# Kernel tuning notes

Measured on AMD Instinct MI355X. Metric: run time of the kernel, lower is better.

The kernel has to match this reference:

```python
import jax, jax.numpy as jnp
import numpy as np
from jax import lax

RATIOS = np.array([0.5, 1.0, 2.0], dtype=np.float32)
SCALES = np.array([8.0, 16.0, 32.0], dtype=np.float32)
BASE = 16.0
FEAT_STRIDE = 16
N_PRE_NMS = 6000
N_POST_NMS = 300
NMS_THRESH = 0.7
MIN_SIZE = 16.0
SCALE = 1.0
NEG_INF = -1e30


def generate_anchor_base():
    # (y1, x1, y2, x2) anchors centered at (BASE/2, BASE/2)
    h = BASE * SCALES[None, :] * np.sqrt(RATIOS)[:, None]          # [3,3]
    w = BASE * SCALES[None, :] * np.sqrt(1.0 / RATIOS)[:, None]
    cy = cx = BASE / 2.0
    ab = np.stack([cy - h / 2, cx - w / 2, cy + h / 2, cx + w / 2], axis=-1)
    return jnp.asarray(ab.reshape(-1, 4), dtype=jnp.float32)       # [9,4]


def enumerate_shift_anchor(anchor_base, hh, ww):
    sy = jnp.arange(hh, dtype=jnp.float32) * FEAT_STRIDE
    sx = jnp.arange(ww, dtype=jnp.float32) * FEAT_STRIDE
    mx, my = jnp.meshgrid(sx, sy)                                   # np.meshgrid(shift_x, shift_y)
    shift = jnp.stack([my.ravel(), mx.ravel(), my.ravel(), mx.ravel()], axis=1)  # [K,4]
    return (shift[:, None, :] + anchor_base[None, :, :]).reshape(-1, 4)          # [K*9,4]


def conv2d(x, w, b, pad):
    y = lax.conv_general_dilated(x, w, (1, 1), [(pad, pad), (pad, pad)],
                                 dimension_numbers=('NCHW', 'OIHW', 'NCHW'))
    return y + b[None, :, None, None]


def loc2bbox(anchor, loc):
    h = anchor[:, 2] - anchor[:, 0]
    w = anchor[:, 3] - anchor[:, 1]
    cy = anchor[:, 0] + 0.5 * h
    cx = anchor[:, 1] + 0.5 * w
    dy, dx, dh, dw = loc[:, 0], loc[:, 1], loc[:, 2], loc[:, 3]
    ncy = dy * h + cy
    ncx = dx * w + cx
    nh = jnp.exp(dh) * h
    nw = jnp.exp(dw) * w
    return jnp.stack([ncy - 0.5 * nh, ncx - 0.5 * nw, ncy + 0.5 * nh, ncx + 0.5 * nw], axis=1)


def nms_fixed(boxes, scores):
    # boxes [P,4] already score-sorted desc; greedy NMS, fixed N_POST_NMS outputs (zero-padded)
    def body(i, state):
        sc, keep = state
        idx = jnp.argmax(sc)
        valid = sc[idx] > NEG_INF / 2
        keep = keep.at[i].set(jnp.where(valid, idx, -1))
        box = boxes[idx]
        tl = jnp.maximum(box[:2], boxes[:, :2])
        br = jnp.minimum(box[2:], boxes[:, 2:])
        wh = jnp.clip(br - tl, 0.0)
        inter = wh[:, 0] * wh[:, 1]
        a1 = (box[2] - box[0]) * (box[3] - box[1])
        a2 = (boxes[:, 2] - boxes[:, 0]) * (boxes[:, 3] - boxes[:, 1])
        iou = inter / jnp.maximum(a1 + a2 - inter, 1e-6)
        sc = jnp.where(iou > NMS_THRESH, NEG_INF, sc)
        sc = sc.at[idx].set(NEG_INF)
        return sc, keep
    keep = jnp.full((N_POST_NMS,), -1, dtype=jnp.int32)
    _, keep = lax.fori_loop(0, N_POST_NMS, body, (scores, keep))
    rois = boxes[jnp.maximum(keep, 0)]
    return jnp.where(keep[:, None] >= 0, rois, 0.0)                # [N_POST,4]


def propose_one(loc, fg_score, anchor, img_h, img_w):
    roi = loc2bbox(anchor, loc)                                     # [A,4]
    roi = jnp.stack([jnp.clip(roi[:, 0], 0.0, img_h),
                     jnp.clip(roi[:, 1], 0.0, img_w),
                     jnp.clip(roi[:, 2], 0.0, img_h),
                     jnp.clip(roi[:, 3], 0.0, img_w)], axis=1)
    min_size = MIN_SIZE * SCALE
    hs = roi[:, 2] - roi[:, 0]
    ws = roi[:, 3] - roi[:, 1]
    valid = (hs >= min_size) & (ws >= min_size)
    sc = jnp.where(valid, fg_score, NEG_INF)
    top_sc, top_idx = lax.top_k(sc, N_PRE_NMS)
    return nms_fixed(roi[top_idx], top_sc)


def reference(x, conv1_w, conv1_b, score_w, score_b, loc_w, loc_b, img_h, img_w):
    n, _, hh, ww = x.shape
    anchor = enumerate_shift_anchor(generate_anchor_base(), hh, ww)  # [hh*ww*9,4]
    n_anchor = anchor.shape[0] // (hh * ww)
    feat = jax.nn.relu(conv2d(x, conv1_w, conv1_b, 1))
    rpn_locs = conv2d(feat, loc_w, loc_b, 0).transpose(0, 2, 3, 1).reshape(n, -1, 4)
    rpn_scores = conv2d(feat, score_w, score_b, 0).transpose(0, 2, 3, 1)
    soft = jax.nn.softmax(rpn_scores.reshape(n, hh, ww, n_anchor, 2), axis=4)
    rpn_fg = soft[..., 1].reshape(n, -1)
    rpn_scores = rpn_scores.reshape(n, -1, 2)
    rois = jax.vmap(lambda l, s: propose_one(l, s, anchor, float(img_h), float(img_w)))(rpn_locs, rpn_fg)
    return rpn_locs, rpn_scores, rois, anchor


def setup_inputs() -> dict:
    key = jax.random.key(0)
    ks = jax.random.split(key, 4)
    return {
        'x': jax.random.normal(ks[0], (4, 512, 64, 64), dtype=jnp.float32),
        'conv1_w': jax.random.normal(ks[1], (512, 512, 3, 3), dtype=jnp.float32) * 0.01,
        'conv1_b': jnp.zeros((512,), dtype=jnp.float32),
        'score_w': jax.random.normal(ks[2], (18, 512, 1, 1), dtype=jnp.float32) * 0.01,
        'score_b': jnp.zeros((18,), dtype=jnp.float32),
        'loc_w': jax.random.normal(ks[3], (36, 512, 1, 1), dtype=jnp.float32) * 0.01,
        'loc_b': jnp.zeros((36,), dtype=jnp.float32),
        'img_h': 1024,
        'img_w': 1024,
    }
```

## Files before the change

### kernel.cpp

```cpp
#include <hip/hip_runtime.h>
#include <stdint.h>

typedef unsigned int u32;
typedef unsigned long long u64;
typedef unsigned short ushort_t;

#define NANCH 36864
#define NPRE 6000
#define NPOST 300
#define CAP 6144
#define NKEEP 6000
#define MROWS 6016
#define MW 192
#define NEG_INF_F (-1e30f)

typedef __attribute__((ext_vector_type(8))) __bf16 bf8_t;
typedef __attribute__((ext_vector_type(8))) unsigned short us8_t;
typedef __attribute__((ext_vector_type(16))) float f32x16;

union pun8 { us8_t u; bf8_t b; };

__device__ __forceinline__ u32 fsort(float f) {
    u32 u = __float_as_uint(f);
    return (u & 0x80000000u) ? ~u : (u | 0x80000000u);
}

__device__ __forceinline__ unsigned short f2bf(float f) {
    u32 u = __float_as_uint(f);
    u32 r = (u + 0x7FFFu + ((u >> 16) & 1u)) >> 16;
    return (unsigned short)r;
}
__device__ __forceinline__ float bf2f(unsigned short s) {
    return __uint_as_float(((u32)s) << 16);
}

__device__ __forceinline__ int ctz32(u32 x) {
    return __builtin_ctz(x ? x : 1u);
}

__global__ void setup_k(const float* __restrict__ w1, const float* __restrict__ sw,
                        const float* __restrict__ lw, ushort_t* __restrict__ Wp,
                        float* __restrict__ wt1, float* __restrict__ out_anchor,
                        u32* __restrict__ cnt) {
    const int bid = blockIdx.x;
    const int tid = threadIdx.x;
    if (bid < 128) {
        int T = bid * 256 + tid;
        int lane31 = T & 31;
        int cot    = (T >> 5) & 15;
        int khalf  = (T >> 9) & 1;
        int kc     = T >> 10;
        int co  = cot * 32 + lane31;
        int ci0 = kc * 16 + khalf * 8;
        int lane = lane31 + khalf * 32;
        const float* wr = w1 + (size_t)co * 4608 + (size_t)ci0 * 9;
        us8_t* P = (us8_t*)Wp;
        const size_t sa_stride = (size_t)9 * 32 * 16 * 64;
#pragma unroll
        for (int t = 0; t < 9; ++t) {
            us8_t vh, vm, vl;
#pragma unroll
            for (int j = 0; j < 8; ++j) {
                float v = wr[j * 9 + t];
                unsigned short h = f2bf(v); float r1 = v - bf2f(h);
                unsigned short m = f2bf(r1); float r2 = r1 - bf2f(m);
                vh[j] = h; vm[j] = m; vl[j] = f2bf(r2);
            }
            size_t base = ((((size_t)t) * 32 + kc) * 16 + cot) * 64 + lane;
            P[base] = vh;
            P[base + sa_stride] = vm;
            P[base + 2 * sa_stride] = vl;
        }
    } else if (bid < 256) {
        int i = (bid - 128) * 256 + tid;
        int ci = i >> 6;
        int ch = i & 63;
        float v = 0.f;
        if (ch < 18) v = sw[ch * 512 + ci];
        else if (ch < 54) v = lw[(ch - 18) * 512 + ci];
        wt1[i] = v;
    } else if (bid < 400) {
        int i = (bid - 256) * 256 + tid;
        if (i < NANCH) {
            int p = i / 9, a = i - p * 9;
            int y = p / 64, xq = p - y * 64;
            int r = a / 3, s = a - r * 3;
            const float rat[3] = {0.5f, 1.f, 2.f};
            const float scl[3] = {8.f, 16.f, 32.f};
            float hh = 16.f * scl[s] * sqrtf(rat[r]);
            float wwv = 16.f * scl[s] * sqrtf(1.f / rat[r]);
            float ab0 = 8.f - 0.5f * hh, ab1 = 8.f - 0.5f * wwv;
            float ab2 = 8.f + 0.5f * hh, ab3 = 8.f + 0.5f * wwv;
            float sy = 16.f * (float)y, sx = 16.f * (float)xq;
            ((float4*)out_anchor)[i] = make_float4(sy + ab0, sx + ab1, sy + ab2, sx + ab3);
        }
    } else {
        if (tid < 8) cnt[tid] = 0u;
    }
}

__global__ __launch_bounds__(256, 2) void conv_mfma_k(const float* __restrict__ x,
                                                      const ushort_t* __restrict__ Wp,
                                                      const float* __restrict__ bias,
                                                      float* __restrict__ feat,
                                                      int img_base) {
    __shared__ __align__(16) unsigned short xs[3 * 6336];

    const int bid = blockIdx.x;
    const int xcd = bid & 7;
    const int rest = bid >> 3;
    const int rest_max = gridDim.x >> 3;
    const int coq = xcd >> 1;
    const int g = (xcd & 1) * rest_max + rest;
    const int fimg = g >> 5;
    const int hp = g & 31;
    const int n = img_base + fimg;
    const int h0 = hp * 2;

    const int tid = threadIdx.x;
    const int lane = tid & 63;
    const int wv = tid >> 6;
    const int r = wv & 1;
    const int coh = (wv >> 1);
    const int col31 = lane & 31;
    const int halfk = lane >> 5;

    f32x16 acc[4];
#pragma unroll
    for (int q = 0; q < 4; ++q)
#pragma unroll
        for (int i = 0; i < 16; ++i) acc[q][i] = 0.f;

    const us8_t* Pw = (const us8_t*)Wp;
    const size_t sa_stride = (size_t)9 * 32 * 16 * 64;
    static const int sal[6] = {0, 0, 1, 0, 1, 2};
    static const int sbl[6] = {0, 1, 0, 2, 1, 0};

    for (int kc = 0; kc < 32; ++kc) {
        for (int e = tid; e < 528; e += 256) {
            int half = e & 1;
            int rc = e >> 1;
            int rr = rc / 66;
            int cc = rc - rr * 66;
            int gr = h0 + rr - 1;
            int gc = cc - 1;
            bool inb = ((unsigned)gr < 64u) && ((unsigned)gc < 64u);
            int ci0 = kc * 16 + half * 8;
            const float* xp = x + ((((size_t)n * 512 + ci0) * 64 + gr) * 64 + gc);
            us8_t vh, vm, vl;
#pragma unroll
            for (int j = 0; j < 8; ++j) {
                float v = inb ? xp[(size_t)j * 4096] : 0.f;
                unsigned short h = f2bf(v); float r1 = v - bf2f(h);
                unsigned short m = f2bf(r1); float r2 = r1 - bf2f(m);
                vh[j] = h; vm[j] = m; vl[j] = f2bf(r2);
            }
            int off = (rr * 66 + cc) * 24 + half * 8;
            *(us8_t*)&xs[off] = vh;
            *(us8_t*)&xs[6336 + off] = vm;
            *(us8_t*)&xs[12672 + off] = vl;
        }
        __syncthreads();

#pragma unroll
        for (int t = 0; t < 9; ++t) {
            const int kh = t / 3, kw = t - kh * 3;
            pun8 Bf[3][2];
            int boff0 = ((r + kh) * 66 + (col31 + kw)) * 24 + halfk * 8;
#pragma unroll
            for (int sb = 0; sb < 3; ++sb)
#pragma unroll
                for (int ps = 0; ps < 2; ++ps)
                    Bf[sb][ps].u = *(const us8_t*)&xs[sb * 6336 + boff0 + ps * (32 * 24)];
            pun8 Af[3][2];
            size_t abase = (((size_t)t * 32 + kc) * 16 + coq * 4 + coh * 2) * 64 + lane;
#pragma unroll
            for (int sa = 0; sa < 3; ++sa)
#pragma unroll
                for (int cs = 0; cs < 2; ++cs)
                    Af[sa][cs].u = Pw[sa * sa_stride + abase + (size_t)cs * 64];
#pragma unroll
            for (int pp = 0; pp < 6; ++pp) {
                const int sa = sal[pp], sb = sbl[pp];
#pragma unroll
                for (int cs = 0; cs < 2; ++cs)
#pragma unroll
                    for (int ps = 0; ps < 2; ++ps)
                        acc[cs * 2 + ps] = __builtin_amdgcn_mfma_f32_32x32x16_bf16(
                            Af[sa][cs].b, Bf[sb][ps].b, acc[cs * 2 + ps], 0, 0, 0);
            }
        }
        __syncthreads();
    }

#pragma unroll
    for (int cs = 0; cs < 2; ++cs)
#pragma unroll
        for (int ps = 0; ps < 2; ++ps)
#pragma unroll
            for (int i = 0; i < 16; ++i) {
                int m = (i & 3) + 8 * (i >> 2) + 4 * halfk;
                int co = coq * 128 + coh * 64 + cs * 32 + m;
                float v = acc[cs * 2 + ps][i] + bias[co];
                v = v > 0.f ? v : 0.f;
                feat[(((size_t)fimg * 512 + co) * 64 + (h0 + r)) * 64 + (ps * 32 + col31)] = v;
            }
}

__global__ __launch_bounds__(64) void head_k(const float* __restrict__ feat,
                                             const float* __restrict__ wt1,
                                             const float* __restrict__ sb,
                                             const float* __restrict__ lb,
                                             const int* __restrict__ img_h,
                                             const int* __restrict__ img_w,
                                             float* __restrict__ out_loc,
                                             float* __restrict__ out_sc,
                                             float* __restrict__ boxes,
                                             float* __restrict__ scf,
                                             int img_base) {
    const int lane = threadIdx.x;
    const int row = blockIdx.x;
    const int fimg = blockIdx.y;
    const int n = img_base + fimg;

    float acc[56];
#pragma unroll
    for (int i = 0; i < 56; i++) acc[i] = 0.f;

    for (int ci = 0; ci < 512; ++ci) {
        float f = feat[(((size_t)fimg * 512 + ci) * 64 + row) * 64 + lane];
        const float4* wp = (const float4*)(wt1 + ci * 64);
#pragma unroll
        for (int q = 0; q < 14; q++) {
            float4 w4 = wp[q];
            acc[q * 4 + 0] = fmaf(f, w4.x, acc[q * 4 + 0]);
            acc[q * 4 + 1] = fmaf(f, w4.y, acc[q * 4 + 1]);
            acc[q * 4 + 2] = fmaf(f, w4.z, acc[q * 4 + 2]);
            acc[q * 4 + 3] = fmaf(f, w4.w, acc[q * 4 + 3]);
        }
    }

    float ihf = (float)img_h[0];
    float iwf = (float)img_w[0];
    int p = row * 64 + lane;
    size_t base = (size_t)n * NANCH + (size_t)p * 9;
    float sy = 16.f * (float)row;
    float sx = 16.f * (float)lane;
    const float rat[3] = {0.5f, 1.f, 2.f};
    const float scl[3] = {8.f, 16.f, 32.f};

#pragma unroll
    for (int a = 0; a < 9; a++) {
        int rr = a / 3, s = a % 3;
        float hh = 16.f * scl[s] * sqrtf(rat[rr]);
        float wwv = 16.f * scl[s] * sqrtf(1.f / rat[rr]);
        float ab0 = 8.f - 0.5f * hh, ab1 = 8.f - 0.5f * wwv;
        float ab2 = 8.f + 0.5f * hh, ab3 = 8.f + 0.5f * wwv;
        float a0 = sy + ab0, a1c = sx + ab1, a2 = sy + ab2, a3 = sx + ab3;

        float s0 = acc[a * 2 + 0] + sb[a * 2 + 0];
        float s1 = acc[a * 2 + 1] + sb[a * 2 + 1];
        ((float2*)out_sc)[base + a] = make_float2(s0, s1);
        float m = fmaxf(s0, s1);
        float e0 = expf(s0 - m), e1 = expf(s1 - m);
        float fg = e1 / (e0 + e1);

        float dy = acc[18 + a * 4 + 0] + lb[a * 4 + 0];
        float dx = acc[18 + a * 4 + 1] + lb[a * 4 + 1];
        float dh = acc[18 + a * 4 + 2] + lb[a * 4 + 2];
        float dw = acc[18 + a * 4 + 3] + lb[a * 4 + 3];
        ((float4*)out_loc)[base + a] = make_float4(dy, dx, dh, dw);

        float h_ = a2 - a0, w_ = a3 - a1c;
        float cy = a0 + 0.5f * h_, cx = a1c + 0.5f * w_;
        float ncy = dy * h_ + cy, ncx = dx * w_ + cx;
        float nh = expf(dh) * h_, nw = expf(dw) * w_;
        float y1 = ncy - 0.5f * nh, x1 = ncx - 0.5f * nw;
        float y2 = ncy + 0.5f * nh, x2 = ncx + 0.5f * nw;
        y1 = fminf(fmaxf(y1, 0.f), ihf);
        x1 = fminf(fmaxf(x1, 0.f), iwf);
        y2 = fminf(fmaxf(y2, 0.f), ihf);
        x2 = fminf(fmaxf(x2, 0.f), iwf);
        float hs = y2 - y1, wsz = x2 - x1;
        bool valid = (hs >= 16.f) && (wsz >= 16.f);
        ((float4*)boxes)[base + a] = make_float4(y1, x1, y2, x2);
        scf[base + a] = valid ? fg : NEG_INF_F;
    }
}

__global__ __launch_bounds__(1024) void radix_k(const float* __restrict__ scf, u32* __restrict__ uT) {
    const int b = blockIdx.x;
    const int tid = threadIdx.x;
    const float* s = scf + (size_t)b * NANCH;
    __shared__ u32 hist[256];
    __shared__ u32 sel_prefix;
    __shared__ int sel_rank;
    if (tid == 0) { sel_prefix = 0u; sel_rank = NPRE; }
    __syncthreads();
    for (int p = 3; p >= 0; --p) {
        for (int i = tid; i < 256; i += 1024) hist[i] = 0u;
        __syncthreads();
        u32 prefix = sel_prefix;
        u32 highmask = (p == 3) ? 0u : (0xFFFFFFFFu << ((p + 1) * 8));
        for (int i = tid; i < NANCH; i += 1024) {
            u32 u = fsort(s[i]);
            if ((u & highmask) == prefix)
                atomicAdd(&hist[(u >> (p * 8)) & 255], 1u);
        }
        __syncthreads();
        if (tid == 0) {
            int r = sel_rank;
            u32 accum = 0;
            int bsel = 0;
            for (int bb = 255; bb >= 0; --bb) {
                accum += hist[bb];
                if ((int)accum >= r) {
                    bsel = bb;
                    sel_rank = r - (int)(accum - hist[bb]);
                    break;
                }
            }
            sel_prefix = prefix | ((u32)bsel << (p * 8));
        }
        __syncthreads();
    }
    if (tid == 0) uT[b] = sel_prefix;
}

__global__ void compact_k(const float* __restrict__ scf, const u32* __restrict__ uT,
                          u32* __restrict__ cnt, u32* __restrict__ cidx) {
    int b = blockIdx.y;
    int i = blockIdx.x * 256 + threadIdx.x;
    float s = scf[(size_t)b * NANCH + i];
    u32 u = fsort(s);
    if (u >= uT[b] && s > -5e29f) {
        u32 p = atomicAdd(&cnt[b], 1u);
        if (p < CAP) cidx[(size_t)b * CAP + p] = (u32)i;
    }
}

__global__ __launch_bounds__(1024) void sort_k(const float* __restrict__ scf,
                                               const float* __restrict__ boxes,
                                               u32* __restrict__ cnt,
                                               const u32* __restrict__ cidx,
                                               float4* __restrict__ sbox) {
    __shared__ u64 sk[8192];
    const int b = blockIdx.x;
    const int tid = threadIdx.x;
    int count = (int)cnt[b];
    if (count > CAP) count = CAP;

    for (int i = tid; i < 8192; i += 1024) {
        u64 key = 0ull;
        if (i < count) {
            u32 idx = cidx[(size_t)b * CAP + i];
            u32 u = fsort(scf[(size_t)b * NANCH + idx]);
            key = ((u64)u << 32) | (u64)(0xFFFFFFFFu - idx);
        }
        sk[i] = key;
    }

    for (int k = 2; k <= 8192; k <<= 1) {
        for (int j = k >> 1; j > 0; j >>= 1) {
            __syncthreads();
            for (int i = tid; i < 8192; i += 1024) {
                int p = i ^ j;
                if (p > i) {
                    bool up = (i & k) == 0;
                    u64 a = sk[i], c = sk[p];
                    bool sw = up ? (a < c) : (a > c);
                    if (sw) { sk[i] = c; sk[p] = a; }
                }
            }
        }
    }
    __syncthreads();

    int S = count < NKEEP ? count : NKEEP;
    if (tid == 0) cnt[4 + b] = (u32)S;
    const float4* Bx = (const float4*)boxes;
    for (int i = tid; i < S; i += 1024) {
        u32 idx = 0xFFFFFFFFu - (u32)(sk[i] & 0xFFFFFFFFull);
        sbox[(size_t)b * CAP + i] = Bx[(size_t)b * NANCH + idx];
    }
}

__global__ __launch_bounds__(256) void mask_k(const float4* __restrict__ sbox,
                                              const u32* __restrict__ cnt,
                                              u32* __restrict__ mask) {
    __shared__ float4 rb[64];
    __shared__ float ra[64];
    const int tile = blockIdx.x;
    const int b = blockIdx.y;
    const int tid = threadIdx.x;
    const int lane = tid & 63;
    const int wv = tid >> 6;
    const int r0 = tile * 64;

    if (tid < 64) {
        float4 v = sbox[(size_t)b * CAP + (r0 + tid)];
        rb[tid] = v;
        ra[tid] = (v.z - v.x) * (v.w - v.y);
    }
    __syncthreads();

    for (int chunk = (tile >> 2); chunk < 24; ++chunk) {
        int c = chunk * 256 + tid;
        float4 cb = sbox[(size_t)b * CAP + c];
        float a2 = (cb.z - cb.x) * (cb.w - cb.y);
        u64 mine = 0ull;
#pragma unroll 4
        for (int r = 0; r < 64; ++r) {
            float4 rr = rb[r];
            float ty = fmaxf(rr.x, cb.x);
            float tx = fmaxf(rr.y, cb.y);
            float by = fminf(rr.z, cb.z);
            float bx = fminf(rr.w, cb.w);
            float ih = fmaxf(by - ty, 0.f);
            float iw = fmaxf(bx - tx, 0.f);
            float inter = ih * iw;
            float iou = inter / fmaxf(ra[r] + a2 - inter, 1e-6f);
            u64 bal = __ballot(iou > 0.7f);
            if (lane == r) mine = bal;
        }
        int row = r0 + lane;
        u64* dst = (u64*)(mask + ((size_t)b * MROWS + row) * MW);
        dst[chunk * 4 + wv] = mine;
    }
}

__global__ __launch_bounds__(1024) void scan_k(const u32* __restrict__ mask,
                                               const float4* __restrict__ sbox,
                                               const u32* __restrict__ cnt,
                                               u32* __restrict__ sink,
                                               float4* __restrict__ out_rois) {
    const int b = blockIdx.x;
    const int tid = threadIdx.x;
    const int wv = tid >> 6;
    const int lane = tid & 63;
    const int S = (int)cnt[4 + b];

    __shared__ int keep[NPOST];
    __shared__ int posS;
    volatile int* vpos = &posS;
    if (tid == 0) *vpos = 0;
    __syncthreads();

    const u32* mbase = mask + (size_t)b * MROWS * MW;

    if (wv == 0) {
        u32 a0, a1, a2v;
        {
            int w;
            w = lane;       a0  = (w * 32 + 32 <= S) ? 0xFFFFFFFFu : ((w * 32 < S) ? ((1u << (S - w * 32)) - 1u) : 0u);
            w = 64 + lane;  a1  = (w * 32 + 32 <= S) ? 0xFFFFFFFFu : ((w * 32 < S) ? ((1u << (S - w * 32)) - 1u) : 0u);
            w = 128 + lane; a2v = (w * 32 + 32 <= S) ? 0xFFFFFFFFu : ((w * 32 < S) ? ((1u << (S - w * 32)) - 1u) : 0u);
        }

        int it = 0;
        while (it < NPOST) {
            int j;
            u64 b0 = __ballot(a0 != 0u);
            if (b0) {
                int L = __builtin_ctzll(b0);
                int cv = (lane << 5) + ctz32(a0);
                j = __shfl(cv, L);
            } else {
                u64 b1 = __ballot(a1 != 0u);
                if (b1) {
                    int L = __builtin_ctzll(b1);
                    int cv = ((64 + lane) << 5) + ctz32(a1);
                    j = __shfl(cv, L);
                } else {
                    u64 b2 = __ballot(a2v != 0u);
                    if (!b2) break;
                    int L = __builtin_ctzll(b2);
                    int cv = ((128 + lane) << 5) + ctz32(a2v);
                    j = __shfl(cv, L);
                }
            }
            if (lane == 0) { keep[it] = j; *vpos = j; }
            ++it;

            int wj = j >> 5;
            u32 bit = 1u << (j & 31);
            if (wj == lane) a0 &= ~bit;
            else if (wj == 64 + lane) a1 &= ~bit;
            else if (wj == 128 + lane) a2v &= ~bit;

            const u32* row = mbase + (size_t)j * MW;
            u32 m0 = row[lane];
            u32 m1 = row[64 + lane];
            u32 m2 = row[128 + lane];
            a0 &= ~m0; a1 &= ~m1; a2v &= ~m2;
        }

        if (lane == 0) *vpos = (1 << 28);

        int total = it;
        for (int i = lane; i < NPOST; i += 64) {
            float4 v = make_float4(0.f, 0.f, 0.f, 0.f);
            if (i < total) v = sbox[(size_t)b * CAP + keep[i]];
            out_rois[(size_t)b * NPOST + i] = v;
        }
    } else {
        u32 dummy = 0u;
        const int W = 2048;
        for (int r = wv - 1; r < MROWS; r += 15) {
            int sp = 0;
            while (*vpos + W <= r && sp < 65536) { __builtin_amdgcn_s_sleep(2); ++sp; }
            if (*vpos >= (1 << 27)) break;
            const u32* row = mbase + (size_t)r * MW;
            dummy += row[lane] + row[64 + lane] + row[128 + lane];
        }
        if (dummy == 0xDEADBEEFu) sink[b] = dummy;
    }
}

extern "C" void kernel_launch(void* const* d_in, const int* in_sizes, int n_in,
                              void* d_out, int out_size, void* d_ws, size_t ws_size,
                              hipStream_t stream) {
    const float* x  = (const float*)d_in[0];
    const float* w1 = (const float*)d_in[1];
    const float* b1 = (const float*)d_in[2];
    const float* sw = (const float*)d_in[3];
    const float* sb = (const float*)d_in[4];
    const float* lw = (const float*)d_in[5];
    const float* lb = (const float*)d_in[6];
    const int* ih   = (const int*)d_in[7];
    const int* iw   = (const int*)d_in[8];
    float* out = (float*)d_out;

    char* ws = (char*)d_ws;
    const size_t FEAT_OFF = 14286848;
    const size_t NEED_BIG = 51413504;
    const bool big = (ws_size >= NEED_BIG);

    ushort_t* Wp  = (ushort_t*)(ws);
    float* feat   = (float*)(ws + FEAT_OFF);
    u32* mask     = (u32*)(ws);
    const size_t RB = big ? (FEAT_OFF + 33554432) : (FEAT_OFF + 16777216);
    float* wt1    = (float*)(ws + RB);
    float* boxes  = (float*)(ws + RB + 131072);
    float* scf    = (float*)(ws + RB + 2490368);
    u32* uT       = (u32*)(ws + RB + 3080192);
    u32* cnt      = (u32*)(ws + RB + 3080448);
    u32* cidx     = (u32*)(ws + RB + 3080704);
    float4* sbox  = (float4*)(ws + RB + 3179008);

    float* out_loc = out;
    float* out_sc  = out + 589824;
    float4* out_roi = (float4*)(out + 884736);
    float* out_anc = out + 889536;

    hipLaunchKernelGGL(setup_k, dim3(401), dim3(256), 0, stream, w1, sw, lw, Wp, wt1, out_anc, cnt);

    if (big) {
        hipLaunchKernelGGL(conv_mfma_k, dim3(512), dim3(256), 0, stream, x, Wp, b1, feat, 0);
        hipLaunchKernelGGL(head_k, dim3(64, 4), dim3(64), 0, stream, feat, wt1, sb, lb, ih, iw,
                           out_loc, out_sc, boxes, scf, 0);
    } else {
        for (int pass = 0; pass < 2; ++pass) {
            hipLaunchKernelGGL(conv_mfma_k, dim3(256), dim3(256), 0, stream, x, Wp, b1, feat, pass * 2);
            hipLaunchKernelGGL(head_k, dim3(64, 2), dim3(64), 0, stream, feat, wt1, sb, lb, ih, iw,
                               out_loc, out_sc, boxes, scf, pass * 2);
        }
    }

    hipLaunchKernelGGL(radix_k, dim3(4), dim3(1024), 0, stream, scf, uT);
    hipLaunchKernelGGL(compact_k, dim3(144, 4), dim3(256), 0, stream, scf, uT, cnt, cidx);
    hipLaunchKernelGGL(sort_k, dim3(4), dim3(1024), 0, stream, scf, boxes, cnt, cidx, sbox);
    hipLaunchKernelGGL(mask_k, dim3(94, 4), dim3(256), 0, stream, sbox, cnt, mask);
    hipLaunchKernelGGL(scan_k, dim3(4), dim3(1024), 0, stream, mask, sbox, cnt, cidx, out_roi);
}
```

Baseline: 1.114 ms.

## Pre-split input to bf16x3 in setup and stream tiles via global_load_lds

Adds a pre-pass in setup_k that converts the fp32 input into three bf16 split planes in a channel-blocked layout stored in workspace. The conv kernel then loads its input tiles straight into LDS with global_load_lds instead of converting them per block, which removes conversion work repeated by the blocks that share each input row. The LDS tile shrinks and halo columns are zeroed once. The cost is an extra workspace pass, a larger workspace requirement that gates the path, and setup blocks that loop serially over 32 row pairs.

```diff
diff --git a/kernel.cpp b/kernel.cpp
--- a/kernel.cpp
+++ b/kernel.cpp
@@ -38,10 +38,20 @@
     return __builtin_ctz(x ? x : 1u);
 }
 
+__device__ __forceinline__ void gl_lds16(const void* g, void* l) {
+    __builtin_amdgcn_global_load_lds(
+        (const __attribute__((address_space(1))) unsigned int*)(g),
+        (__attribute__((address_space(3))) unsigned int*)(l), 16, 0, 0);
+}
+
+#define XS_SPL ((size_t)4 * 32 * 64 * 2 * 64)
+
 __global__ void setup_k(const float* __restrict__ w1, const float* __restrict__ sw,
-                        const float* __restrict__ lw, ushort_t* __restrict__ Wp,
+                        const float* __restrict__ lw, const float* __restrict__ x,
+                        ushort_t* __restrict__ Wp, ushort_t* __restrict__ Xs,
                         float* __restrict__ wt1, float* __restrict__ out_anchor,
                         u32* __restrict__ cnt) {
+    __shared__ float xt[16][2][64];
     const int bid = blockIdx.x;
     const int tid = threadIdx.x;
     if (bid < 128) {
@@ -94,17 +104,152 @@
             float sy = 16.f * (float)y, sx = 16.f * (float)xq;
             ((float4*)out_anchor)[i] = make_float4(sy + ab0, sx + ab1, sy + ab2, sx + ab3);
         }
+    } else if (bid == 400) {
+        if (tid < 8) cnt[tid] = 0u;
     } else {
-        if (tid < 8) cnt[tid] = 0u;
-    }
-}
-
-__global__ __launch_bounds__(256, 2) void conv_mfma_k(const float* __restrict__ x,
+        int pk = bid - 401;
+        int img = pk >> 5, kc = pk & 31;
+        us8_t* XP = (us8_t*)Xs;
+        for (int h2 = 0; h2 < 32; ++h2) {
+#pragma unroll
+            for (int i = 0; i < 8; ++i) {
+                int idx = i * 256 + tid;
+                int ci = idx >> 7, rem = idx & 127, hrow = rem >> 6, w = rem & 63;
+                int h = h2 * 2 + hrow;
+                xt[ci][hrow][w] = x[(((size_t)img * 512 + kc * 16 + ci) * 64 + h) * 64 + w];
+            }
+            __syncthreads();
+            {
+                int hrow = tid >> 7, st = tid & 127, half = st >> 6, w = st & 63;
+                int h = h2 * 2 + hrow;
+                us8_t vh, vm, vl;
+#pragma unroll
+                for (int j = 0; j < 8; ++j) {
+                    float v = xt[half * 8 + j][hrow][w];
+                    unsigned short hb = f2bf(v); float r1 = v - bf2f(hb);
+                    unsigned short mb = f2bf(r1); float r2 = r1 - bf2f(mb);
+                    vh[j] = hb; vm[j] = mb; vl[j] = f2bf(r2);
+                }
+                size_t ob = ((((size_t)img * 32 + kc) * 64 + h) * 2 + half) * 64 + w;
+                XP[ob] = vh;
+                XP[XS_SPL + ob] = vm;
+                XP[2 * XS_SPL + ob] = vl;
+            }
+            __syncthreads();
+        }
+    }
+}
+
+__global__ __launch_bounds__(256, 2) void conv_mfma_k(const ushort_t* __restrict__ Xs,
                                                       const ushort_t* __restrict__ Wp,
                                                       const float* __restrict__ bias,
-                                                      float* __restrict__ feat,
-                                                      int img_base) {
-    __shared__ __align__(16) unsigned short xs[3 * 6336];
+                                                      float* __restrict__ feat) {
+    __shared__ __align__(16) unsigned short xs[12672];
+
+    const int bid = blockIdx.x;
+    const int xcd = bid & 7;
+    const int rest = bid >> 3;
+    const int coq = xcd >> 1;
+    const int g = (xcd & 1) * 64 + rest;
+    const int fimg = g >> 5;
+    const int hp = g & 31;
+    const int h0 = hp * 2;
+
+    const int tid = threadIdx.x;
+    const int lane = tid & 63;
+    const int wv = tid >> 6;
+    const int r = wv & 1;
+    const int coh = (wv >> 1);
+    const int col31 = lane & 31;
+    const int halfk = lane >> 5;
+
+    {
+        u32* p = (u32*)xs;
+        for (int i = tid; i < 6336; i += 256) p[i] = 0u;
+    }
+    __syncthreads();
+
+    f32x16 acc[4];
+#pragma unroll
+    for (int q = 0; q < 4; ++q)
+#pragma unroll
+        for (int i = 0; i < 16; ++i) acc[q][i] = 0.f;
+
+    const us8_t* Pw = (const us8_t*)Wp;
+    const size_t sa_stride = (size_t)9 * 32 * 16 * 64;
+    static const int sal[6] = {0, 0, 1, 0, 1, 2};
+    static const int sbl[6] = {0, 1, 0, 2, 1, 0};
+
+    for (int kc = 0; kc < 32; ++kc) {
+#pragma unroll
+        for (int q = 0; q < 6; ++q) {
+            int i = wv * 6 + q;
+            int split = i >> 3;
+            int rem = i & 7;
+            int rr = rem >> 1;
+            int half = rem & 1;
+            int gh = h0 + rr - 1;
+            if ((unsigned)gh < 64u) {
+                const char* src = (const char*)Xs +
+                    (((((size_t)split * 4 + fimg) * 32 + kc) * 64 + gh) * 2 + half) * 1024 +
+                    (size_t)lane * 16;
+                void* dst = (void*)&xs[(((split * 2 + half) * 4 + rr) * 66 + 1) * 8];
+                gl_lds16(src, dst);
+            }
+        }
+        __syncthreads();
+
+#pragma unroll
+        for (int t = 0; t < 9; ++t) {
+            const int kh = t / 3, kw = t - kh * 3;
+            pun8 Bf[3][2];
+#pragma unroll
+            for (int sb = 0; sb < 3; ++sb)
+#pragma unroll
+                for (int ps = 0; ps < 2; ++ps)
+                    Bf[sb][ps].u = *(const us8_t*)&xs[(((sb * 2 + halfk) * 4 + (r + kh)) * 66 +
+                                                      (ps * 32 + col31 + kw)) * 8];
+            pun8 Af[3][2];
+            size_t abase = (((size_t)t * 32 + kc) * 16 + coq * 4 + coh * 2) * 64 + lane;
+#pragma unroll
+            for (int sa = 0; sa < 3; ++sa)
+#pragma unroll
+                for (int cs = 0; cs < 2; ++cs)
+                    Af[sa][cs].u = Pw[sa * sa_stride + abase + (size_t)cs * 64];
+#pragma unroll
+            for (int pp = 0; pp < 6; ++pp) {
+                const int sa = sal[pp], sb = sbl[pp];
+#pragma unroll
+                for (int cs = 0; cs < 2; ++cs)
+#pragma unroll
+                    for (int ps = 0; ps < 2; ++ps)
+                        acc[cs * 2 + ps] = __builtin_amdgcn_mfma_f32_32x32x16_bf16(
+                            Af[sa][cs].b, Bf[sb][ps].b, acc[cs * 2 + ps], 0, 0, 0);
+            }
+        }
+        __syncthreads();
+    }
+
+#pragma unroll
+    for (int cs = 0; cs < 2; ++cs)
+#pragma unroll
+        for (int ps = 0; ps < 2; ++ps)
+#pragma unroll
+            for (int i = 0; i < 16; ++i) {
+                int m = (i & 3) + 8 * (i >> 2) + 4 * halfk;
+                int co = coq * 128 + coh * 64 + cs * 32 + m;
+                float v = acc[cs * 2 + ps][i] + bias[co];
+                v = v > 0.f ? v : 0.f;
+                feat[(((size_t)fimg * 512 + co) * 64 + (h0 + r)) * 64 + (ps * 32 + col31)] = v;
+            }
+}
+
+__global__ __launch_bounds__(256, 2) void conv_fb_k(const float* __restrict__ x,
+                                                    const ushort_t* __restrict__ Wp,
+                                                    const float* __restrict__ bias,
+                                                    float* __restrict__ feat,
+                                                    int img_base) {
+    __shared__ __align__(16) unsigned short xsb[3 * 6336];
 
     const int bid = blockIdx.x;
     const int xcd = bid & 7;
@@ -156,9 +301,9 @@
                 vh[j] = h; vm[j] = m; vl[j] = f2bf(r2);
             }
             int off = (rr * 66 + cc) * 24 + half * 8;
-            *(us8_t*)&xs[off] = vh;
-            *(us8_t*)&xs[6336 + off] = vm;
-            *(us8_t*)&xs[12672 + off] = vl;
+            *(us8_t*)&xsb[off] = vh;
+            *(us8_t*)&xsb[6336 + off] = vm;
+            *(us8_t*)&xsb[12672 + off] = vl;
         }
         __syncthreads();
 
@@ -171,7 +316,7 @@
             for (int sb = 0; sb < 3; ++sb)
 #pragma unroll
                 for (int ps = 0; ps < 2; ++ps)
-                    Bf[sb][ps].u = *(const us8_t*)&xs[sb * 6336 + boff0 + ps * (32 * 24)];
+                    Bf[sb][ps].u = *(const us8_t*)&xsb[sb * 6336 + boff0 + ps * (32 * 24)];
             pun8 Af[3][2];
             size_t abase = (((size_t)t * 32 + kc) * 16 + coq * 4 + coh * 2) * 64 + lane;
 #pragma unroll
@@ -532,14 +677,15 @@
     float* out = (float*)d_out;
 
     char* ws = (char*)d_ws;
-    const size_t FEAT_OFF = 14286848;
+    const size_t NEED_XL  = 101614080;
     const size_t NEED_BIG = 51413504;
-    const bool big = (ws_size >= NEED_BIG);
+    const int mode = (ws_size >= NEED_XL) ? 2 : (ws_size >= NEED_BIG ? 1 : 0);
 
     ushort_t* Wp  = (ushort_t*)(ws);
-    float* feat   = (float*)(ws + FEAT_OFF);
+    ushort_t* Xs  = (ushort_t*)(ws + 14155776);
+    float* feat   = (float*)(ws + (mode == 2 ? 64487424 : 14286848));
     u32* mask     = (u32*)(ws);
-    const size_t RB = big ? (FEAT_OFF + 33554432) : (FEAT_OFF + 16777216);
+    const size_t RB = (mode == 2) ? 98041856 : (mode == 1 ? 47841280 : 31064064);
     float* wt1    = (float*)(ws + RB);
     float* boxes  = (float*)(ws + RB + 131072);
     float* scf    = (float*)(ws + RB + 2490368);
@@ -553,15 +699,20 @@
     float4* out_roi = (float4*)(out + 884736);
     float* out_anc = out + 889536;
 
-    hipLaunchKernelGGL(setup_k, dim3(401), dim3(256), 0, stream, w1, sw, lw, Wp, wt1, out_anc, cnt);
-
-    if (big) {
-        hipLaunchKernelGGL(conv_mfma_k, dim3(512), dim3(256), 0, stream, x, Wp, b1, feat, 0);
+    hipLaunchKernelGGL(setup_k, dim3(mode == 2 ? 529 : 401), dim3(256), 0, stream,
+                       w1, sw, lw, x, Wp, Xs, wt1, out_anc, cnt);
+
+    if (mode == 2) {
+        hipLaunchKernelGGL(conv_mfma_k, dim3(512), dim3(256), 0, stream, (const ushort_t*)Xs, Wp, b1, feat);
+        hipLaunchKernelGGL(head_k, dim3(64, 4), dim3(64), 0, stream, feat, wt1, sb, lb, ih, iw,
+                           out_loc, out_sc, boxes, scf, 0);
+    } else if (mode == 1) {
+        hipLaunchKernelGGL(conv_fb_k, dim3(512), dim3(256), 0, stream, x, Wp, b1, feat, 0);
         hipLaunchKernelGGL(head_k, dim3(64, 4), dim3(64), 0, stream, feat, wt1, sb, lb, ih, iw,
                            out_loc, out_sc, boxes, scf, 0);
     } else {
         for (int pass = 0; pass < 2; ++pass) {
-            hipLaunchKernelGGL(conv_mfma_k, dim3(256), dim3(256), 0, stream, x, Wp, b1, feat, pass * 2);
+            hipLaunchKernelGGL(conv_fb_k, dim3(256), dim3(256), 0, stream, x, Wp, b1, feat, pass * 2);
             hipLaunchKernelGGL(head_k, dim3(64, 2), dim3(64), 0, stream, feat, wt1, sb, lb, ih, iw,
                                out_loc, out_sc, boxes, scf, pass * 2);
         }
```

Result: no change. 1.118 ms (+0.3%).
